# Kernel tuning notes

Measured on AMD Instinct MI355X. Metric: run time of the kernel, lower is better.

Reference implementation:

```python
import jax, jax.numpy as jnp
import numpy as np
from jax import lax

IN_CH = 256
UP = 8
DN = ('NCHW', 'OIHW', 'NCHW')


def setup_inputs() -> dict:
    key = jax.random.key(0)
    ks = jax.random.split(key, 6)
    B, H, W = 8, 96, 96
    flow_lr = jax.random.normal(ks[0], (B, 2, H, W), dtype=jnp.float32)
    feat = jax.random.normal(ks[1], (B, IN_CH, H, W), dtype=jnp.float32)
    w1 = jax.random.normal(ks[2], (IN_CH, IN_CH, 3, 3), dtype=jnp.float32) * 0.02
    b1 = jnp.zeros((IN_CH,), dtype=jnp.float32)
    w2 = jax.random.normal(ks[3], (UP * UP * 9, IN_CH, 1, 1), dtype=jnp.float32) * 0.02
    b2 = jnp.zeros((UP * UP * 9,), dtype=jnp.float32)
    return {"flow_lr": flow_lr, "feat": feat, "w1": w1, "b1": b1, "w2": w2, "b2": b2}


def reference(flow_lr, feat, w1, b1, w2, b2):
    B, _, H, W = flow_lr.shape
    up = UP
    # mask head: 3x3 conv + relu + 1x1 conv
    x = lax.conv_general_dilated(feat, w1, (1, 1), 'SAME', dimension_numbers=DN)
    x = jax.nn.relu(x + b1[None, :, None, None])
    mask = lax.conv_general_dilated(x, w2, (1, 1), 'SAME', dimension_numbers=DN)
    mask = mask + b2[None, :, None, None]
    # channel dim 9*up*up splits as (9, up, up), matching torch .view(B,1,9,up,up,H,W)
    mask = mask.reshape(B, 9, up, up, H, W)
    mask = jax.nn.softmax(mask, axis=1)
    # unfold(flow_lr, 3, padding=1): 9 zero-padded 3x3 shifts, row-major (kh, kw)
    pad = jnp.pad(flow_lr, ((0, 0), (0, 0), (1, 1), (1, 1)))
    flow_unf = jnp.stack(
        [pad[:, :, i:i + H, j:j + W] for i in range(3) for j in range(3)], axis=2
    )  # (B, 2, 9, H, W)
    # convex combination over the 9 neighbors
    up_flow = jnp.einsum('bkpqhw,bckhw->bcpqhw', mask, flow_unf)  # (B,2,up,up,H,W)
    # pixel-shuffle: (B,2,p,q,H,W) -> (B,2,H,p,W,q) -> (B,2,H*up,W*up)
    up_flow = up_flow.transpose(0, 1, 4, 2, 5, 3).reshape(B, 2, H * up, W * up)
    return up_flow * up
```

## Files before the change

### kernel.cpp

```cpp
#include <hip/hip_runtime.h>
#include <hip/hip_bf16.h>
#include <stdint.h>

typedef unsigned short u16;
typedef __bf16 bf16x8 __attribute__((ext_vector_type(8)));
typedef float f32x4 __attribute__((ext_vector_type(4)));

#define MFMA16(a, b, c) __builtin_amdgcn_mfma_f32_16x16x32_bf16((a), (b), (c), 0, 0, 0)

#define GLOAD16(g, l)                                                        \
  __builtin_amdgcn_global_load_lds(                                          \
      (const __attribute__((address_space(1))) void*)(g),                    \
      (__attribute__((address_space(3))) void*)(l), 16, 0, 0)

static __device__ __forceinline__ u16 f2bf(float f) {
  union { float f; uint32_t u; } v;
  v.f = f;
  uint32_t u = v.u;
  return (u16)((u + 0x7FFFu + ((u >> 16) & 1u)) >> 16);
}
static __device__ __forceinline__ float u2f(uint32_t u) {
  union { uint32_t u; float f; } v;
  v.u = u;
  return v.f;
}

#define FEATT_ELEMS (8u * 98u * 98u * 256u)
#define W1T_OFF     FEATT_ELEMS
#define W1T_ELEMS   (256u * 2304u)
#define W2B_OFF     (W1T_OFF + W1T_ELEMS)
#define W2B_ELEMS   (576u * 256u)
#define X_OFF       (W2B_OFF + W2B_ELEMS)

__global__ __launch_bounds__(256) void prep_all(const float* __restrict__ feat,
                                                const float* __restrict__ w1,
                                                const float* __restrict__ w2,
                                                u16* __restrict__ featT,
                                                u16* __restrict__ w1t,
                                                u16* __restrict__ w2b) {
  const int blk = blockIdx.x;
  const int t = threadIdx.x;
  if (blk < 388) {
    int tid = blk * 256 + t;
    int b = tid / (388 * 32);
    int rem = tid % (388 * 32);
    int pos = rem >> 5, v = rem & 31;
    int h, w;
    if (pos < 98) { h = 0; w = pos; }
    else if (pos < 196) { h = 97; w = pos - 98; }
    else if (pos < 292) { h = pos - 196 + 1; w = 0; }
    else { h = pos - 292 + 1; w = 97; }
    uint4* dst = (uint4*)(featT + (size_t)((b * 98 + h) * 98 + w) * 256 + v * 8);
    *dst = make_uint4(0, 0, 0, 0);
  } else if (blk < 4996) {
    int idx = blk - 388;
    int pt = idx % 144, ct = (idx / 144) & 3, b = idx / 576;
    const int p0 = pt * 64, c0 = ct * 64;
    __shared__ float tile[64][65];
    const int pj = t & 63, ci0 = t >> 6;
#pragma unroll
    for (int r = 0; r < 16; ++r) {
      int ci = r * 4 + ci0;
      tile[ci][pj] = feat[(b * 256 + c0 + ci) * 9216 + p0 + pj];
    }
    __syncthreads();
    const int pl = t >> 2, cc0 = (t & 3) * 16;
    const int pix = p0 + pl;
    const int h = pix / 96, w = pix % 96;
    uint32_t u[8];
#pragma unroll
    for (int i = 0; i < 8; ++i) {
      u16 lo = f2bf(tile[cc0 + 2 * i][pl]);
      u16 hi = f2bf(tile[cc0 + 2 * i + 1][pl]);
      u[i] = (uint32_t)lo | ((uint32_t)hi << 16);
    }
    uint4* dst = (uint4*)(featT + (size_t)((b * 98 + h + 1) * 98 + (w + 1)) * 256 + c0 + cc0);
    dst[0] = make_uint4(u[0], u[1], u[2], u[3]);
    dst[1] = make_uint4(u[4], u[5], u[6], u[7]);
  } else {
    int i = (blk - 4996) * 256 + t;
    if (i < 589824) {
      int oc = i / 2304, r = i % 2304;
      int tap = r >> 8, cin = r & 255;
      w1t[i] = f2bf(w1[(oc * 256 + cin) * 9 + tap]);
    } else {
      int j = i - 589824;
      if (j < 147456) w2b[j] = f2bf(w2[j]);
    }
  }
}

__global__ __launch_bounds__(512, 4) void gemm1(const u16* __restrict__ featT,
                                                const u16* __restrict__ w1t,
                                                const float* __restrict__ b1,
                                                u16* __restrict__ xout) {
  __shared__ __align__(16) u16 sA[128 * 64];
  __shared__ __align__(16) u16 sB[256 * 64];
  __shared__ float sb1[256];

  const int t = threadIdx.x;
  const int wave = t >> 6, lane = t & 63;
  const int bid = blockIdx.x;
  const int mt = (bid & 7) * 72 + (bid >> 3);
  const int b = mt / 72;
  const int ip0 = (mt % 72) * 128;

  if (t < 256) sb1[t] = b1[t];

  const u16* aBase[2];
  const u16* bBase[4];
#pragma unroll
  for (int r = 0; r < 2; ++r) {
    int row = r * 64 + wave * 8 + (lane >> 3);
    int chunk = (lane & 7) ^ (row & 7);
    int ip = ip0 + row;
    int h = ip / 96, w = ip % 96;
    aBase[r] = featT + (size_t)((b * 98 + h + 1) * 98 + (w + 1)) * 256 + chunk * 8;
  }
#pragma unroll
  for (int r = 0; r < 4; ++r) {
    int row = wave * 32 + r * 8 + (lane >> 3);
    int chunk = (lane & 7) ^ (row & 7);
    bBase[r] = w1t + (size_t)row * 2304 + chunk * 8;
  }

  const int wm = wave >> 2, wn = wave & 3;
  int aoffs[4][2], boffs[4][2];
#pragma unroll
  for (int m = 0; m < 4; ++m) {
#pragma unroll
    for (int ki = 0; ki < 2; ++ki) {
      int kc = ki * 4 + (lane >> 4);
      int rowa = wm * 64 + m * 16 + (lane & 15);
      aoffs[m][ki] = rowa * 64 + ((kc ^ (rowa & 7)) * 8);
      int rowb = wn * 64 + m * 16 + (lane & 15);
      boffs[m][ki] = rowb * 64 + ((kc ^ (rowb & 7)) * 8);
    }
  }

  f32x4 acc[4][4];
#pragma unroll
  for (int m = 0; m < 4; ++m)
#pragma unroll
    for (int n = 0; n < 4; ++n) acc[m][n] = f32x4{0.f, 0.f, 0.f, 0.f};

  for (int kt = 0; kt < 36; ++kt) {
    int tap = kt >> 2;
    int dh = tap / 3 - 1, dw = tap % 3 - 1;
    int aoff = (dh * 98 + dw) * 256 + (kt & 3) * 64;
    int boff = kt * 64;
#pragma unroll
    for (int r = 0; r < 2; ++r) GLOAD16(aBase[r] + aoff, &sA[(r * 64 + wave * 8) * 64]);
#pragma unroll
    for (int r = 0; r < 4; ++r) GLOAD16(bBase[r] + boff, &sB[(wave * 32 + r * 8) * 64]);
    __syncthreads();
#pragma unroll
    for (int ki = 0; ki < 2; ++ki) {
      bf16x8 av[4], bv[4];
#pragma unroll
      for (int m = 0; m < 4; ++m) av[m] = *(const bf16x8*)&sA[aoffs[m][ki]];
#pragma unroll
      for (int n = 0; n < 4; ++n) bv[n] = *(const bf16x8*)&sB[boffs[n][ki]];
#pragma unroll
      for (int m = 0; m < 4; ++m)
#pragma unroll
        for (int n = 0; n < 4; ++n) acc[m][n] = MFMA16(av[m], bv[n], acc[m][n]);
    }
    __syncthreads();
  }

  const int pix0g = mt * 128;
#pragma unroll
  for (int m = 0; m < 4; ++m) {
    int pixl = wm * 64 + m * 16 + ((lane >> 4) << 2);
#pragma unroll
    for (int n = 0; n < 4; ++n) {
      int oc = wn * 64 + n * 16 + (lane & 15);
      float bias = sb1[oc];
      f32x4 v = acc[m][n];
#pragma unroll
      for (int j = 0; j < 4; ++j) {
        float val = v[j] + bias;
        val = val > 0.f ? val : 0.f;
        xout[(size_t)(pix0g + pixl + j) * 256 + oc] = f2bf(val);
      }
    }
  }
}

__global__ __launch_bounds__(512) void gemm2fq(const u16* __restrict__ xws,
                                               const u16* __restrict__ w2b,
                                               const float* __restrict__ b2g,
                                               const float* __restrict__ flow,
                                               float* __restrict__ out) {
  __shared__ __align__(16) u16 sW[2][9216];
  __shared__ uint32_t sFlowP[1152];
  __shared__ float sb2f[576];

  const int t = threadIdx.x;
  const int wave = t >> 6, lane = t & 63;
  const int bid = blockIdx.x;
  const int mt = (bid & 7) * 72 + (bid >> 3);
  const int b = mt / 72;
  const int ipl0 = (mt % 72) * 128;
  const int l15 = lane & 15, kc = lane >> 4;

  auto stageQ = [&](int u, int bufi) {
    int cI = u >> 2, kq = u & 3;
    if (t < 384) {
#pragma unroll
      for (int pass = 0; pass < 3; ++pass) {
        int c = pass * 384 + t;
        int n = c >> 3, cl = c & 7;
        int cg = cl ^ (n & 7);
        int chan = (n >> 4) * 64 + cI * 16 + (n & 15);
        GLOAD16(w2b + (size_t)chan * 256 + kq * 64 + cg * 8,
                &sW[bufi][(pass * 384 + wave * 64) * 8]);
      }
    }
  };
  stageQ(0, 0);

  for (int i = t; i < 1152; i += 512) {
    int nf = i >> 7, p = i & 127;
    int ip = ipl0 + p;
    int h = ip / 96, w = ip % 96;
    int hh = h + nf / 3 - 1, ww = w + nf % 3 - 1;
    float vx = 0.f, vy = 0.f;
    if (hh >= 0 && hh < 96 && ww >= 0 && ww < 96) {
      vx = flow[b * 18432 + hh * 96 + ww];
      vy = flow[b * 18432 + 9216 + hh * 96 + ww];
    }
    sFlowP[i] = (uint32_t)f2bf(vx) | ((uint32_t)f2bf(vy) << 16);
  }
  for (int i = t; i < 576; i += 512) sb2f[i] = b2g[i];

  const int px = wave * 16 + l15;
  const u16* xr = &xws[((size_t)mt * 128 + px) * 256];
  bf16x8 areg[8];
#pragma unroll
  for (int s = 0; s < 8; ++s) areg[s] = *(const bf16x8*)&xr[(s * 4 + kc) * 8];

  const int iph = (ipl0 + px) / 96, ipw = (ipl0 + px) % 96;
  const size_t ob = ((size_t)(b * 2) * 768 + iph * 8) * 768 + ipw * 8;
  const int q0 = (kc & 1) * 4, pk = kc >> 1;

  uint32_t fp[9];
  f32x4 acc[9];
#pragma unroll
  for (int u = 0; u < 16; ++u) {
    __syncthreads();
    if (u == 0) {
#pragma unroll
      for (int nf = 0; nf < 9; ++nf) fp[nf] = sFlowP[nf * 128 + px];
    }
    if (u < 15) stageQ(u + 1, (u + 1) & 1);
    const int cI = u >> 2, kq = u & 3;
    if (kq == 0) {
#pragma unroll
      for (int nf = 0; nf < 9; ++nf) acc[nf] = f32x4{0.f, 0.f, 0.f, 0.f};
    }
    const u16* base = sW[u & 1];
    __builtin_amdgcn_s_setprio(1);
#pragma unroll
    for (int ki = 0; ki < 2; ++ki) {
      bf16x8 a = areg[kq * 2 + ki];
      int kcc = ki * 4 + kc;
#pragma unroll
      for (int nf = 0; nf < 9; ++nf) {
        int n = nf * 16 + l15;
        bf16x8 wv = *(const bf16x8*)&base[n * 64 + ((kcc ^ (n & 7)) * 8)];
        acc[nf] = MFMA16(wv, a, acc[nf]);
      }
    }
    __builtin_amdgcn_s_setprio(0);
    if (kq == 3) {
      f32x4 vx4, vy4;
#pragma unroll
      for (int j = 0; j < 4; ++j) {
        int pql = kc * 4 + j;
        float ssum = 0.f, fx = 0.f, fy = 0.f;
#pragma unroll
        for (int nf = 0; nf < 9; ++nf) {
          float e = __expf(acc[nf][j] + sb2f[nf * 64 + cI * 16 + pql]);
          ssum += e;
          fx += e * u2f(fp[nf] << 16);
          fy += e * u2f(fp[nf] & 0xFFFF0000u);
        }
        float sc = 8.0f / ssum;
        vx4[j] = fx * sc;
        vy4[j] = fy * sc;
      }
      int p = cI * 2 + pk;
      *(f32x4*)&out[ob + (size_t)p * 768 + q0] = vx4;
      *(f32x4*)&out[ob + 589824 + (size_t)p * 768 + q0] = vy4;
    }
  }
}

extern "C" void kernel_launch(void* const* d_in, const int* in_sizes, int n_in,
                              void* d_out, int out_size, void* d_ws, size_t ws_size,
                              hipStream_t stream) {
  const float* flow = (const float*)d_in[0];
  const float* feat = (const float*)d_in[1];
  const float* w1 = (const float*)d_in[2];
  const float* b1 = (const float*)d_in[3];
  const float* w2 = (const float*)d_in[4];
  const float* b2 = (const float*)d_in[5];
  float* out = (float*)d_out;
  u16* ws = (u16*)d_ws;
  u16* featT = ws;
  u16* w1t = ws + W1T_OFF;
  u16* w2b = ws + W2B_OFF;
  u16* xws = ws + X_OFF;

  prep_all<<<7876, 256, 0, stream>>>(feat, w1, w2, featT, w1t, w2b);
  gemm1<<<576, 512, 0, stream>>>(featT, w1t, b1, xws);
  gemm2fq<<<576, 512, 0, stream>>>(xws, w2b, b2, flow, out);
}
```

Measured before the change: 183.9 us.

## Read 1x1-conv weights directly from global memory instead of LDS staging

The second GEMM kernel no longer double-buffers w2 tiles into LDS with async global-to-LDS loads and per-step barriers. Each lane now loads weight fragments straight from global memory, relying on cache reuse across blocks. The block shrinks from 128 to 64 pixels and from 512 to 256 threads, with twice as many blocks. This removes 16 barriers and the LDS staging, but adds global/L2 load latency inside the MFMA loop and drops the swizzled LDS reuse.

Measured after the change: 310.8 us. 1.69x slower.

```diff
diff --git a/kernel.cpp b/kernel.cpp
--- a/kernel.cpp
+++ b/kernel.cpp
@@ -188,41 +188,24 @@
   }
 }
 
-__global__ __launch_bounds__(512) void gemm2fq(const u16* __restrict__ xws,
-                                               const u16* __restrict__ w2b,
-                                               const float* __restrict__ b2g,
-                                               const float* __restrict__ flow,
-                                               float* __restrict__ out) {
-  __shared__ __align__(16) u16 sW[2][9216];
-  __shared__ uint32_t sFlowP[1152];
+__global__ __launch_bounds__(256) void gemm2g(const u16* __restrict__ xws,
+                                              const u16* __restrict__ w2b,
+                                              const float* __restrict__ b2g,
+                                              const float* __restrict__ flow,
+                                              float* __restrict__ out) {
+  __shared__ uint32_t sFlowP[576];
   __shared__ float sb2f[576];
 
   const int t = threadIdx.x;
   const int wave = t >> 6, lane = t & 63;
   const int bid = blockIdx.x;
-  const int mt = (bid & 7) * 72 + (bid >> 3);
-  const int b = mt / 72;
-  const int ipl0 = (mt % 72) * 128;
+  const int mt = (bid & 7) * 144 + (bid >> 3);
+  const int b = mt / 144;
+  const int ipl0 = (mt % 144) * 64;
   const int l15 = lane & 15, kc = lane >> 4;
 
-  auto stageQ = [&](int u, int bufi) {
-    int cI = u >> 2, kq = u & 3;
-    if (t < 384) {
-#pragma unroll
-      for (int pass = 0; pass < 3; ++pass) {
-        int c = pass * 384 + t;
-        int n = c >> 3, cl = c & 7;
-        int cg = cl ^ (n & 7);
-        int chan = (n >> 4) * 64 + cI * 16 + (n & 15);
-        GLOAD16(w2b + (size_t)chan * 256 + kq * 64 + cg * 8,
-                &sW[bufi][(pass * 384 + wave * 64) * 8]);
-      }
-    }
-  };
-  stageQ(0, 0);
-
-  for (int i = t; i < 1152; i += 512) {
-    int nf = i >> 7, p = i & 127;
+  for (int i = t; i < 576; i += 256) {
+    int nf = i >> 6, p = i & 63;
     int ip = ipl0 + p;
     int h = ip / 96, w = ip % 96;
     int hh = h + nf / 3 - 1, ww = w + nf % 3 - 1;
@@ -232,11 +215,11 @@
       vy = flow[b * 18432 + 9216 + hh * 96 + ww];
     }
     sFlowP[i] = (uint32_t)f2bf(vx) | ((uint32_t)f2bf(vy) << 16);
-  }
-  for (int i = t; i < 576; i += 512) sb2f[i] = b2g[i];
+    sb2f[i] = b2g[i];
+  }
 
   const int px = wave * 16 + l15;
-  const u16* xr = &xws[((size_t)mt * 128 + px) * 256];
+  const u16* xr = &xws[(size_t)(b * 9216 + ipl0 + px) * 256];
   bf16x8 areg[8];
 #pragma unroll
   for (int s = 0; s < 8; ++s) areg[s] = *(const bf16x8*)&xr[(s * 4 + kc) * 8];
@@ -245,56 +228,53 @@
   const size_t ob = ((size_t)(b * 2) * 768 + iph * 8) * 768 + ipw * 8;
   const int q0 = (kc & 1) * 4, pk = kc >> 1;
 
+  __syncthreads();
+
   uint32_t fp[9];
-  f32x4 acc[9];
-#pragma unroll
-  for (int u = 0; u < 16; ++u) {
-    __syncthreads();
-    if (u == 0) {
-#pragma unroll
-      for (int nf = 0; nf < 9; ++nf) fp[nf] = sFlowP[nf * 128 + px];
-    }
-    if (u < 15) stageQ(u + 1, (u + 1) & 1);
-    const int cI = u >> 2, kq = u & 3;
-    if (kq == 0) {
-#pragma unroll
-      for (int nf = 0; nf < 9; ++nf) acc[nf] = f32x4{0.f, 0.f, 0.f, 0.f};
-    }
-    const u16* base = sW[u & 1];
-    __builtin_amdgcn_s_setprio(1);
-#pragma unroll
-    for (int ki = 0; ki < 2; ++ki) {
-      bf16x8 a = areg[kq * 2 + ki];
-      int kcc = ki * 4 + kc;
+#pragma unroll
+  for (int nf = 0; nf < 9; ++nf) fp[nf] = sFlowP[nf * 64 + px];
+
+  const u16* wr[9];
+#pragma unroll
+  for (int nf = 0; nf < 9; ++nf) wr[nf] = w2b + (size_t)(nf * 64 + l15) * 256;
+
+  for (int cI = 0; cI < 4; ++cI) {
+    f32x4 acc[9];
+#pragma unroll
+    for (int nf = 0; nf < 9; ++nf) acc[nf] = f32x4{0.f, 0.f, 0.f, 0.f};
+    const int co = cI * 16 * 256;
+#pragma unroll
+    for (int kq = 0; kq < 4; ++kq) {
+#pragma unroll
+      for (int ki = 0; ki < 2; ++ki) {
+        bf16x8 a = areg[kq * 2 + ki];
+        const int ko = kq * 64 + (ki * 4 + kc) * 8;
+#pragma unroll
+        for (int nf = 0; nf < 9; ++nf) {
+          bf16x8 wv = *(const bf16x8*)&wr[nf][co + ko];
+          acc[nf] = MFMA16(wv, a, acc[nf]);
+        }
+      }
+    }
+    f32x4 vx4, vy4;
+#pragma unroll
+    for (int j = 0; j < 4; ++j) {
+      int pql = kc * 4 + j;
+      float ssum = 0.f, fx = 0.f, fy = 0.f;
 #pragma unroll
       for (int nf = 0; nf < 9; ++nf) {
-        int n = nf * 16 + l15;
-        bf16x8 wv = *(const bf16x8*)&base[n * 64 + ((kcc ^ (n & 7)) * 8)];
-        acc[nf] = MFMA16(wv, a, acc[nf]);
+        float e = __expf(acc[nf][j] + sb2f[nf * 64 + cI * 16 + pql]);
+        ssum += e;
+        fx += e * u2f(fp[nf] << 16);
+        fy += e * u2f(fp[nf] & 0xFFFF0000u);
       }
-    }
-    __builtin_amdgcn_s_setprio(0);
-    if (kq == 3) {
-      f32x4 vx4, vy4;
-#pragma unroll
-      for (int j = 0; j < 4; ++j) {
-        int pql = kc * 4 + j;
-        float ssum = 0.f, fx = 0.f, fy = 0.f;
-#pragma unroll
-        for (int nf = 0; nf < 9; ++nf) {
-          float e = __expf(acc[nf][j] + sb2f[nf * 64 + cI * 16 + pql]);
-          ssum += e;
-          fx += e * u2f(fp[nf] << 16);
-          fy += e * u2f(fp[nf] & 0xFFFF0000u);
-        }
-        float sc = 8.0f / ssum;
-        vx4[j] = fx * sc;
-        vy4[j] = fy * sc;
-      }
-      int p = cI * 2 + pk;
-      *(f32x4*)&out[ob + (size_t)p * 768 + q0] = vx4;
-      *(f32x4*)&out[ob + 589824 + (size_t)p * 768 + q0] = vy4;
-    }
+      float sc = 8.0f / ssum;
+      vx4[j] = fx * sc;
+      vy4[j] = fy * sc;
+    }
+    int p = cI * 2 + pk;
+    *(f32x4*)&out[ob + (size_t)p * 768 + q0] = vx4;
+    *(f32x4*)&out[ob + 589824 + (size_t)p * 768 + q0] = vy4;
   }
 }
 
@@ -316,5 +296,5 @@
 
   prep_all<<<7876, 256, 0, stream>>>(feat, w1, w2, featT, w1t, w2b);
   gemm1<<<576, 512, 0, stream>>>(featT, w1t, b1, xws);
-  gemm2fq<<<576, 512, 0, stream>>>(xws, w2b, b2, flow, out);
-}
+  gemm2g<<<1152, 256, 0, stream>>>(xws, w2b, b2, flow, out);
+}
```
